# Kernel tuning notes

Hardware: AMD Instinct MI355X
Metric: run time of the kernel (lower is better)

The kernel has to match this reference:

```python
import jax, jax.numpy as jnp
import numpy as np

B, NUM_RX, NUM_CHIRPS, SAMPLES = 16, 4, 64, 256
D_BINS, R_BINS = 64, 256


def _conv3d(x, w, b, pad):
    y = jax.lax.conv_general_dilated(x, w, (1, 1, 1), pad,
                                     dimension_numbers=('NCDHW', 'OIDHW', 'NCDHW'))
    return y + b[None, :, None, None, None]


def _conv2d(x, w, b, pad):
    y = jax.lax.conv_general_dilated(x, w, (1, 1), pad,
                                     dimension_numbers=('NCHW', 'OIHW', 'NCHW'))
    return y + b[None, :, None, None]


def _bn2(x, s, t):
    return x * s[None, :, None, None] + t[None, :, None, None]


def _bn3(x, s, t):
    return x * s[None, :, None, None, None] + t[None, :, None, None, None]


def _upsample_bilinear_ac(x, oh, ow):
    # torch Upsample(mode='bilinear', align_corners=True)
    _, _, h, w = x.shape
    ph = jnp.linspace(0.0, h - 1.0, oh)
    pw = jnp.linspace(0.0, w - 1.0, ow)
    h0 = jnp.clip(jnp.floor(ph).astype(jnp.int32), 0, h - 1)
    h1 = jnp.clip(h0 + 1, 0, h - 1)
    fh = ph - h0
    w0 = jnp.clip(jnp.floor(pw).astype(jnp.int32), 0, w - 1)
    w1 = jnp.clip(w0 + 1, 0, w - 1)
    fw = pw - w0
    x = x[:, :, h0, :] * (1.0 - fh)[None, None, :, None] + x[:, :, h1, :] * fh[None, None, :, None]
    x = x[:, :, :, w0] * (1.0 - fw) + x[:, :, :, w1] * fw
    return x


def setup_inputs() -> dict:
    ks = iter(jax.random.split(jax.random.key(0), 80))

    def nrm(shape, s=0.05):
        return s * jax.random.normal(next(ks), shape, dtype=jnp.float32)

    inp = {'x': jax.random.normal(next(ks), (B, NUM_RX, NUM_CHIRPS, SAMPLES, 2), dtype=jnp.float32)}

    def conv(name, shape):
        inp[name + '_w'] = nrm(shape)
        inp[name + '_b'] = nrm((shape[0],))

    def bn(name, n):  # BatchNorm in inference form folded to scale/shift
        inp[name + '_s'] = 1.0 + nrm((n,), 0.1)
        inp[name + '_t'] = nrm((n,), 0.1)

    conv('tc1', (16, 2, 1, 1, 3)); bn('tc1', 16)
    conv('tc2', (32, 16, 1, 1, 3)); bn('tc2', 32)
    conv('rx', (32, 32, NUM_RX, 1, 1)); bn('rx', 32)
    conv('cc1', (64, 32 * NUM_CHIRPS, 3, 3)); bn('cc1', 64)
    conv('cc2', (64, 64, 3, 3)); bn('cc2', 64)
    conv('rd1', (128, 64, 3, 3)); bn('rd1', 128)
    conv('rd2', (128, 128, 3, 3)); bn('rd2', 128)
    conv('up1', (64, 128, 3, 3)); bn('up1', 64)
    conv('up2', (32, 64, 3, 3)); bn('up2', 32)
    conv('up3', (1, 32, 1, 1))
    inp['wr'] = jax.random.normal(next(ks), (SAMPLES, R_BINS, 2), dtype=jnp.float32)
    inp['wd'] = jax.random.normal(next(ks), (NUM_CHIRPS, D_BINS, 2), dtype=jnp.float32)
    return inp


def reference(x, tc1_w, tc1_b, tc1_s, tc1_t, tc2_w, tc2_b, tc2_s, tc2_t,
              rx_w, rx_b, rx_s, rx_t, cc1_w, cc1_b, cc1_s, cc1_t,
              cc2_w, cc2_b, cc2_s, cc2_t, rd1_w, rd1_b, rd1_s, rd1_t,
              rd2_w, rd2_b, rd2_s, rd2_t, up1_w, up1_b, up1_s, up1_t,
              up2_w, up2_b, up2_s, up2_t, up3_w, up3_b, wr, wd):
    r = jax.nn.relu
    p3 = [(0, 0), (0, 0), (1, 1)]
    p2 = [(1, 1), (1, 1)]
    h = jnp.transpose(x, (0, 4, 1, 2, 3))                      # [B,2,RX,C,S]
    h = r(_bn3(_conv3d(h, tc1_w, tc1_b, p3), tc1_s, tc1_t))
    h = r(_bn3(_conv3d(h, tc2_w, tc2_b, p3), tc2_s, tc2_t))
    h = r(_bn3(_conv3d(h, rx_w, rx_b, [(0, 0)] * 3), rx_s, rx_t))[:, :, 0]  # [B,32,C,S]
    h = h.reshape(h.shape[0], -1, SAMPLES)[:, :, None, :]      # [B,32*C,1,S]
    h = r(_bn2(_conv2d(h, cc1_w, cc1_b, p2), cc1_s, cc1_t))
    h = r(_bn2(_conv2d(h, cc2_w, cc2_b, p2), cc2_s, cc2_t))
    h = r(_bn2(_conv2d(h, rd1_w, rd1_b, p2), rd1_s, rd1_t))
    h = r(_bn2(_conv2d(h, rd2_w, rd2_b, p2), rd2_s, rd2_t))
    h = _upsample_bilinear_ac(h, D_BINS, R_BINS)               # [B,128,D,R]
    h = r(_bn2(_conv2d(h, up1_w, up1_b, p2), up1_s, up1_t))
    h = r(_bn2(_conv2d(h, up2_w, up2_b, p2), up2_s, up2_t))
    h = jax.nn.sigmoid(_conv2d(h, up3_w, up3_b, [(0, 0), (0, 0)]))  # [B,1,D,R]
    # learnable_fft (input is real: x_imag = 0), loops -> two batched matmuls
    xr = h[:, 0]                                               # [B,D,R]
    rr = jnp.einsum('bcs,sr->bcr', xr, wr[:, :, 0])            # range DFT, real
    ri = jnp.einsum('bcs,sr->bcr', xr, wr[:, :, 1])            # range DFT, imag
    rdr = jnp.einsum('bcr,cd->bdr', rr, wd[:, :, 0]) - jnp.einsum('bcr,cd->bdr', ri, wd[:, :, 1])
    rdi = jnp.einsum('bcr,cd->bdr', rr, wd[:, :, 1]) + jnp.einsum('bcr,cd->bdr', ri, wd[:, :, 0])
    mag = jnp.sqrt(rdr * rdr + rdi * rdi) / (NUM_CHIRPS * SAMPLES)
    out = jnp.clip(h + 0.1 * mag[:, None], 0.0, 1.0)
    return jnp.transpose(out, (0, 2, 3, 1))                    # [B,D,R,1]
```

## Files before the change

kernel.cpp:

```cpp
#include <hip/hip_runtime.h>
#include <math.h>

#define OFF_A      0u
#define OFF_P      8388608u
#define OFF_WCC1   10485760u
#define OFF_BCC1   11010048u
#define OFF_WCC2   11010112u
#define OFF_BCC2   11026496u
#define OFF_WRD1   11026560u
#define OFF_BRD1   11059328u
#define OFF_WRD2   11059456u
#define OFF_BRD2   11124992u
#define OFF_WUP1   11125120u
#define OFF_BUP1   11223424u
#define OFF_WUP2   11223488u
#define OFF_BUP2   11346368u
#define OFF_WRX    11346400u
#define OFF_W1F    11350496u
#define OFF_B1F    11350592u
#define OFF_W2F    11350608u
#define OFF_B2F    11352144u
#define OFF_BRXF   11352176u
#define OFF_RP0    0u
#define OFF_RP1    524288u
#define OFF_H      1048576u

__device__ __forceinline__ void fma4(float4& a, const float4& x, float w) {
  a.x = fmaf(x.x, w, a.x); a.y = fmaf(x.y, w, a.y);
  a.z = fmaf(x.z, w, a.z); a.w = fmaf(x.w, w, a.w);
}

__global__ __launch_bounds__(256) void k_repack_front(
    const float* __restrict__ tc1_w, const float* __restrict__ tc1_b, const float* __restrict__ tc1_s, const float* __restrict__ tc1_t,
    const float* __restrict__ tc2_w, const float* __restrict__ tc2_b, const float* __restrict__ tc2_s, const float* __restrict__ tc2_t,
    const float* __restrict__ rx_w, const float* __restrict__ rx_b, const float* __restrict__ rx_s, const float* __restrict__ rx_t,
    float* __restrict__ ws)
{
  const int tid = blockIdx.x * blockDim.x + threadIdx.x;
  const int nth = gridDim.x * blockDim.x;
  for (int i = tid; i < 96; i += nth) ws[OFF_W1F + i] = tc1_w[i] * tc1_s[i/6];
  for (int i = tid; i < 16; i += nth) ws[OFF_B1F + i] = tc1_b[i]*tc1_s[i] + tc1_t[i];
  for (int i = tid; i < 1536; i += nth) {
    int oc = i & 31, r = i >> 5, k = r % 3, ic = r / 3;
    ws[OFF_W2F + i] = tc2_w[oc*48 + ic*3 + k] * tc2_s[oc];
  }
  for (int i = tid; i < 32; i += nth) ws[OFF_B2F + i] = tc2_b[i]*tc2_s[i] + tc2_t[i];
  for (int i = tid; i < 4096; i += nth) {
    int oc = i & 31, ic = (i >> 5) & 31, rxi = i >> 10;
    ws[OFF_WRX + i] = rx_w[(oc*32 + ic)*4 + rxi] * rx_s[oc];
  }
  for (int i = tid; i < 32; i += nth) ws[OFF_BRXF + i] = rx_b[i]*rx_s[i] + rx_t[i];
}

__global__ __launch_bounds__(256, 4) void k_front(
    const float* __restrict__ x, const float* __restrict__ ws_c, float* __restrict__ ws,
    const float* __restrict__ cc1_w, const float* __restrict__ cc1_b, const float* __restrict__ cc1_s, const float* __restrict__ cc1_t,
    const float* __restrict__ cc2_w, const float* __restrict__ cc2_b, const float* __restrict__ cc2_s, const float* __restrict__ cc2_t,
    const float* __restrict__ rd1_w, const float* __restrict__ rd1_b, const float* __restrict__ rd1_s, const float* __restrict__ rd1_t,
    const float* __restrict__ rd2_w, const float* __restrict__ rd2_b, const float* __restrict__ rd2_s, const float* __restrict__ rd2_t,
    const float* __restrict__ up1_w, const float* __restrict__ up1_b, const float* __restrict__ up1_s, const float* __restrict__ up1_t,
    const float* __restrict__ up2_w, const float* __restrict__ up2_b, const float* __restrict__ up2_s, const float* __restrict__ up2_t,
    float* __restrict__ A)
{
  __shared__ float t1s[16][258];
  const int tid = threadIdx.x;

  if (blockIdx.x < 64) {
    const int t = blockIdx.x * 256 + tid;
    const int nth = 64 * 256;
    for (int i = t; i < 2048*64*4; i += nth) {
      int k = i & 3, oc = (i >> 2) & 63, c2 = i >> 8;
      ws[OFF_WCC1 + i] = (k < 3) ? cc1_w[((oc*2048 + c2)*3 + 1)*3 + k] * cc1_s[oc] : 0.f;
    }
    for (int i = t; i < 64; i += nth) ws[OFF_BCC1 + i] = cc1_b[i]*cc1_s[i] + cc1_t[i];
    for (int i = t; i < 64*64; i += nth) {
      int oc = i & 63, ic = i >> 6;
      float4 v;
      v.x = cc2_w[(oc*64 + ic)*9 + 3] * cc2_s[oc];
      v.y = cc2_w[(oc*64 + ic)*9 + 4] * cc2_s[oc];
      v.z = cc2_w[(oc*64 + ic)*9 + 5] * cc2_s[oc];
      v.w = 0.f;
      ((float4*)(ws + OFF_WCC2))[i] = v;
    }
    for (int i = t; i < 64; i += nth) ws[OFF_BCC2 + i] = cc2_b[i]*cc2_s[i] + cc2_t[i];
    for (int i = t; i < 64*128; i += nth) {
      int oc = i & 127, ic = i >> 7;
      float4 v;
      v.x = rd1_w[(oc*64 + ic)*9 + 3] * rd1_s[oc];
      v.y = rd1_w[(oc*64 + ic)*9 + 4] * rd1_s[oc];
      v.z = rd1_w[(oc*64 + ic)*9 + 5] * rd1_s[oc];
      v.w = 0.f;
      ((float4*)(ws + OFF_WRD1))[i] = v;
    }
    for (int i = t; i < 128; i += nth) ws[OFF_BRD1 + i] = rd1_b[i]*rd1_s[i] + rd1_t[i];
    for (int i = t; i < 128*128; i += nth) {
      int oc = i & 127, ic = i >> 7;
      float4 v;
      v.x = rd2_w[(oc*128 + ic)*9 + 3] * rd2_s[oc];
      v.y = rd2_w[(oc*128 + ic)*9 + 4] * rd2_s[oc];
      v.z = rd2_w[(oc*128 + ic)*9 + 5] * rd2_s[oc];
      v.w = 0.f;
      ((float4*)(ws + OFF_WRD2))[i] = v;
    }
    for (int i = t; i < 128; i += nth) ws[OFF_BRD2 + i] = rd2_b[i]*rd2_s[i] + rd2_t[i];
    for (int i = t; i < 3*128*64; i += nth) {
      int oc = i & 63, ic = (i >> 6) & 127, v = i >> 13;
      const int m = (v == 0) ? 6 : (v == 1) ? 7 : 3;
      float4 o = make_float4(0.f, 0.f, 0.f, 0.f);
      for (int kh = 0; kh < 3; ++kh)
        if ((m >> kh) & 1) {
          o.x += up1_w[((oc*128 + ic)*3 + kh)*3 + 0];
          o.y += up1_w[((oc*128 + ic)*3 + kh)*3 + 1];
          o.z += up1_w[((oc*128 + ic)*3 + kh)*3 + 2];
        }
      o.x *= up1_s[oc]; o.y *= up1_s[oc]; o.z *= up1_s[oc];
      ((float4*)(ws + OFF_WUP1))[i] = o;
    }
    for (int i = t; i < 64; i += nth) ws[OFF_BUP1 + i] = up1_b[i]*up1_s[i] + up1_t[i];
    for (int i = t; i < 5*3*64*32; i += nth) {
      int oc = i & 31, ic = (i >> 5) & 63, tt = i >> 11;
      int src = tt % 3, v = tt / 3;
      const int MASKS[15] = {2,4,0,  1,6,0,  0,7,0,  0,3,4,  0,1,2};
      const int m = MASKS[v*3 + src];
      float4 o = make_float4(0.f, 0.f, 0.f, 0.f);
      for (int kh = 0; kh < 3; ++kh)
        if ((m >> kh) & 1) {
          o.x += up2_w[((oc*64 + ic)*3 + kh)*3 + 0];
          o.y += up2_w[((oc*64 + ic)*3 + kh)*3 + 1];
          o.z += up2_w[((oc*64 + ic)*3 + kh)*3 + 2];
        }
      o.x *= up2_s[oc]; o.y *= up2_s[oc]; o.z *= up2_s[oc];
      ((float4*)(ws + OFF_WUP2))[i] = o;
    }
    for (int i = t; i < 32; i += nth) ws[OFF_BUP2 + i] = up2_b[i]*up2_s[i] + up2_t[i];
    return;
  }

  const int bb = blockIdx.x - 64;
  const int b = bb >> 6, chirp = bb & 63;
  const int s = tid;

  if (tid < 32) { int o = tid & 15; int c = (tid >> 4) ? 257 : 0; t1s[o][c] = 0.f; }

  const float* w1f  = ws_c + OFF_W1F;
  const float* b1f  = ws_c + OFF_B1F;
  const float* w2f  = ws_c + OFF_W2F;
  const float* b2f  = ws_c + OFF_B2F;
  const float* wrxf = ws_c + OFF_WRX;
  const float* brxf = ws_c + OFF_BRXF;

  float acc[32];
  #pragma unroll
  for (int j = 0; j < 32; ++j) acc[j] = 0.f;

  #pragma unroll 1
  for (int rxi = 0; rxi < 4; ++rxi) {
    {
      const float2* xb2 = (const float2*)(x + ((size_t)(((b*4 + rxi)*64 + chirp)*256) << 1));
      float2 xm = xb2[s];
      float2 xl = xb2[(s == 0) ? 0 : (s - 1)];
      float2 xr = xb2[(s == 255) ? 255 : (s + 1)];
      if (s == 0)   { xl.x = 0.f; xl.y = 0.f; }
      if (s == 255) { xr.x = 0.f; xr.y = 0.f; }
      #pragma unroll 4
      for (int o = 0; o < 16; ++o) {
        const float* w = w1f + o*6;
        float v = b1f[o];
        v = fmaf(xl.x, w[0], v);
        v = fmaf(xm.x, w[1], v);
        v = fmaf(xr.x, w[2], v);
        v = fmaf(xl.y, w[3], v);
        v = fmaf(xm.y, w[4], v);
        v = fmaf(xr.y, w[5], v);
        t1s[o][s+1] = fmaxf(v, 0.f);
      }
    }
    __syncthreads();

    float t2[32];
    #pragma unroll
    for (int j = 0; j < 32; ++j) t2[j] = b2f[j];
    #pragma unroll 2
    for (int ic = 0; ic < 16; ++ic) {
      float tl = t1s[ic][s];
      float tm = t1s[ic][s+1];
      float tr = t1s[ic][s+2];
      const float* w = w2f + ic*96;
      #pragma unroll
      for (int oc = 0; oc < 32; ++oc)
        t2[oc] = fmaf(tl, w[oc], fmaf(tm, w[32+oc], fmaf(tr, w[64+oc], t2[oc])));
    }
    #pragma unroll
    for (int j = 0; j < 32; ++j) t2[j] = fmaxf(t2[j], 0.f);

    const float* wr0 = wrxf + rxi*1024;
    #pragma unroll 4
    for (int ic = 0; ic < 32; ++ic) {
      float tv = t2[ic];
      const float* w = wr0 + ic*32;
      #pragma unroll
      for (int oc = 0; oc < 32; ++oc)
        acc[oc] = fmaf(tv, w[oc], acc[oc]);
    }
    __syncthreads();
  }

  #pragma unroll 4
  for (int oc = 0; oc < 32; ++oc) {
    float v = fmaxf(acc[oc] + brxf[oc], 0.f);
    A[(size_t)((b*2048 + oc*64 + chirp)*256) + s] = v;
  }
}

__global__ __launch_bounds__(256) void k_cc1(
    const float* __restrict__ A, const float* __restrict__ wp, float* __restrict__ P)
{
  __shared__ __align__(16) float As[256][36];
  const int tid = threadIdx.x;
  const int ks = blockIdx.x & 7;
  const int stile = (blockIdx.x >> 3) & 7;
  const int b = blockIdx.x >> 6;
  const int s0 = stile * 32;
  const int oc = tid & 63;
  const int sg = tid >> 6;
  const int cbase = ks * 256;
  const float4* w4 = (const float4*)wp;

  for (int i = tid; i < 256*36; i += 256) {
    int c = i / 36, si = i - c*36;
    int sA = s0 - 1 + si;
    float v = 0.f;
    if (si < 34 && sA >= 0 && sA < 256)
      v = A[(size_t)(b*2048 + cbase + c)*256 + sA];
    As[c][si] = v;
  }
  __syncthreads();

  const int sb = sg * 8;
  float4 acc0 = make_float4(0.f,0.f,0.f,0.f);
  float4 acc1 = make_float4(0.f,0.f,0.f,0.f);
  #pragma unroll 4
  for (int c = 0; c < 256; ++c) {
    float4 w = w4[(size_t)(cbase + c)*64 + oc];
    float4 a0 = *(const float4*)&As[c][sb];
    float4 a1 = *(const float4*)&As[c][sb + 4];
    float2 a2 = *(const float2*)&As[c][sb + 8];
    acc0.x = fmaf(a0.x,w.x, fmaf(a0.y,w.y, fmaf(a0.z,w.z, acc0.x)));
    acc0.y = fmaf(a0.y,w.x, fmaf(a0.z,w.y, fmaf(a0.w,w.z, acc0.y)));
    acc0.z = fmaf(a0.z,w.x, fmaf(a0.w,w.y, fmaf(a1.x,w.z, acc0.z)));
    acc0.w = fmaf(a0.w,w.x, fmaf(a1.x,w.y, fmaf(a1.y,w.z, acc0.w)));
    acc1.x = fmaf(a1.x,w.x, fmaf(a1.y,w.y, fmaf(a1.z,w.z, acc1.x)));
    acc1.y = fmaf(a1.y,w.x, fmaf(a1.z,w.y, fmaf(a1.w,w.z, acc1.y)));
    acc1.z = fmaf(a1.z,w.x, fmaf(a1.w,w.y, fmaf(a2.x,w.z, acc1.z)));
    acc1.w = fmaf(a1.w,w.x, fmaf(a2.x,w.y, fmaf(a2.y,w.z, acc1.w)));
  }
  float* Pk = P + ((size_t)(ks*16 + b)*256)*64;
  int s = s0 + sb;
  Pk[(size_t)(s+0)*64 + oc] = acc0.x;
  Pk[(size_t)(s+1)*64 + oc] = acc0.y;
  Pk[(size_t)(s+2)*64 + oc] = acc0.z;
  Pk[(size_t)(s+3)*64 + oc] = acc0.w;
  Pk[(size_t)(s+4)*64 + oc] = acc1.x;
  Pk[(size_t)(s+5)*64 + oc] = acc1.y;
  Pk[(size_t)(s+6)*64 + oc] = acc1.z;
  Pk[(size_t)(s+7)*64 + oc] = acc1.w;
}

__global__ __launch_bounds__(256) void k_mid(
    const float* __restrict__ P, const float* __restrict__ bcc1,
    const float* __restrict__ wcc2, const float* __restrict__ bcc2,
    const float* __restrict__ wrd1, const float* __restrict__ brd1,
    const float* __restrict__ wrd2, const float* __restrict__ brd2,
    float* __restrict__ Rp0, float* __restrict__ Rp1)
{
  __shared__ __align__(16) float c1s[64][20];
  __shared__ __align__(16) float c2s[64][20];
  __shared__ __align__(16) float r1s[64][12];
  const int tid = threadIdx.x;
  const int half = blockIdx.x & 1;
  const int stile = (blockIdx.x >> 1) & 31;
  const int b = blockIdx.x >> 6;
  const int s0 = stile * 8;
  const float4* wc2 = (const float4*)wcc2;
  const float4* wr1 = (const float4*)wrd1;
  const float4* wr2 = (const float4*)wrd2;

  for (int i = tid; i < 14*64; i += 256) {
    int ic = i & 63, si = i >> 6;
    int sA = s0 - 3 + si;
    float v = 0.f;
    if (sA >= 0 && sA < 256) {
      float a = bcc1[ic];
      #pragma unroll
      for (int ksp = 0; ksp < 8; ++ksp)
        a += P[((size_t)(ksp*16 + b)*256 + sA)*64 + ic];
      v = fmaxf(a, 0.f);
    }
    c1s[ic][si] = v;
  }
  __syncthreads();

  {
    const int g = tid >> 6, oc = tid & 63;
    if (g < 3) {
      float bb = bcc2[oc];
      float4 acc = make_float4(bb, bb, bb, bb);
      #pragma unroll 4
      for (int ic = 0; ic < 64; ++ic) {
        float4 w = wc2[ic*64 + oc];
        float4 ca = *(const float4*)&c1s[ic][g*4];
        float2 cb = *(const float2*)&c1s[ic][g*4 + 4];
        acc.x = fmaf(ca.x,w.x, fmaf(ca.y,w.y, fmaf(ca.z,w.z, acc.x)));
        acc.y = fmaf(ca.y,w.x, fmaf(ca.z,w.y, fmaf(ca.w,w.z, acc.y)));
        acc.z = fmaf(ca.z,w.x, fmaf(ca.w,w.y, fmaf(cb.x,w.z, acc.z)));
        acc.w = fmaf(ca.w,w.x, fmaf(cb.x,w.y, fmaf(cb.y,w.z, acc.w)));
      }
      float r[4] = {acc.x, acc.y, acc.z, acc.w};
      #pragma unroll
      for (int j = 0; j < 4; ++j) {
        int si = g*4 + j, sA = s0 - 2 + si;
        c2s[oc][si] = (sA >= 0 && sA < 256) ? fmaxf(r[j], 0.f) : 0.f;
      }
    } else {
      int oc2 = tid - 192;
      c2s[oc2][12] = 0.f;
      c2s[oc2][13] = 0.f;
    }
  }
  __syncthreads();

  {
    const int g = tid >> 6, ocl = tid & 63;
    if (g < 3) {
      const int ocg = half*64 + ocl;
      float bb = brd1[ocg];
      float4 acc = make_float4(bb, bb, bb, bb);
      #pragma unroll 4
      for (int ic = 0; ic < 64; ++ic) {
        float4 w = wr1[ic*128 + ocg];
        float4 ca = *(const float4*)&c2s[ic][g*4];
        float2 cb = *(const float2*)&c2s[ic][g*4 + 4];
        acc.x = fmaf(ca.x,w.x, fmaf(ca.y,w.y, fmaf(ca.z,w.z, acc.x)));
        acc.y = fmaf(ca.y,w.x, fmaf(ca.z,w.y, fmaf(ca.w,w.z, acc.y)));
        acc.z = fmaf(ca.z,w.x, fmaf(ca.w,w.y, fmaf(cb.x,w.z, acc.z)));
        acc.w = fmaf(ca.w,w.x, fmaf(cb.x,w.y, fmaf(cb.y,w.z, acc.w)));
      }
      float r[4] = {acc.x, acc.y, acc.z, acc.w};
      #pragma unroll
      for (int j = 0; j < 4; ++j) {
        int si = g*4 + j, sA = s0 - 1 + si;
        if (si < 10)
          r1s[ocl][si] = (sA >= 0 && sA < 256) ? fmaxf(r[j], 0.f) : 0.f;
      }
    } else {
      int oc2 = tid - 192;
      r1s[oc2][10] = 0.f;
      r1s[oc2][11] = 0.f;
    }
  }
  __syncthreads();

  {
    const int g = tid >> 7, oc = tid & 127;
    float bb = half ? 0.f : brd2[oc];
    float4 acc = make_float4(bb, bb, bb, bb);
    #pragma unroll 4
    for (int ic = 0; ic < 64; ++ic) {
      float4 w = wr2[(half*64 + ic)*128 + oc];
      float4 ca = *(const float4*)&r1s[ic][g*4];
      float2 cb = *(const float2*)&r1s[ic][g*4 + 4];
      acc.x = fmaf(ca.x,w.x, fmaf(ca.y,w.y, fmaf(ca.z,w.z, acc.x)));
      acc.y = fmaf(ca.y,w.x, fmaf(ca.z,w.y, fmaf(ca.w,w.z, acc.y)));
      acc.z = fmaf(ca.z,w.x, fmaf(ca.w,w.y, fmaf(cb.x,w.z, acc.z)));
      acc.w = fmaf(ca.w,w.x, fmaf(cb.x,w.y, fmaf(cb.y,w.z, acc.w)));
    }
    float* Rp = half ? Rp1 : Rp0;
    int s = s0 + g*4;
    Rp[((size_t)b*256 + s+0)*128 + oc] = acc.x;
    Rp[((size_t)b*256 + s+1)*128 + oc] = acc.y;
    Rp[((size_t)b*256 + s+2)*128 + oc] = acc.z;
    Rp[((size_t)b*256 + s+3)*128 + oc] = acc.w;
  }
}

__global__ __launch_bounds__(192) void k_up(
    const float* __restrict__ Rp0, const float* __restrict__ Rp1,
    const float* __restrict__ wup1, const float* __restrict__ bup1,
    const float* __restrict__ wup2, const float* __restrict__ bup2,
    const float* __restrict__ up3_w, const float* __restrict__ up3_b,
    float* __restrict__ H)
{
  __shared__ __align__(16) float Rs[128][12];
  __shared__ __align__(16) float u1s[3][64][12];
  __shared__ float u2s[5][32][9];
  const int tid = threadIdx.x;
  const int b = blockIdx.x >> 5;
  const int s0 = (blockIdx.x & 31) * 8;

  for (int i = tid; i < 128*12; i += 192) {
    int ic = i & 127, si = i >> 7;
    int sA = s0 - 2 + si;
    float v = 0.f;
    if (sA >= 0 && sA < 256) {
      size_t idx = ((size_t)b*256 + sA)*128 + ic;
      v = fmaxf(Rp0[idx] + Rp1[idx], 0.f);
    }
    Rs[ic][si] = v;
  }
  __syncthreads();

  {
    const int vi = tid >> 6, oc = tid & 63;
    const float4* w4 = (const float4*)wup1;
    float a[10];
    float bb = bup1[oc];
    #pragma unroll
    for (int p = 0; p < 10; ++p) a[p] = bb;
    #pragma unroll 4
    for (int ic = 0; ic < 128; ++ic) {
      float4 w = w4[(vi*128 + ic)*64 + oc];
      float4 ra = *(const float4*)&Rs[ic][0];
      float4 rb = *(const float4*)&Rs[ic][4];
      float4 rc = *(const float4*)&Rs[ic][8];
      float r[12] = {ra.x,ra.y,ra.z,ra.w, rb.x,rb.y,rb.z,rb.w, rc.x,rc.y,rc.z,rc.w};
      #pragma unroll
      for (int p = 0; p < 10; ++p)
        a[p] = fmaf(r[p],w.x, fmaf(r[p+1],w.y, fmaf(r[p+2],w.z, a[p])));
    }
    #pragma unroll
    for (int p = 0; p < 10; ++p) {
      int sA = s0 - 1 + p;
      u1s[vi][oc][p] = (sA >= 0 && sA < 256) ? fmaxf(a[p], 0.f) : 0.f;
    }
    u1s[vi][oc][10] = 0.f; u1s[vi][oc][11] = 0.f;
  }
  __syncthreads();

  if (tid < 160) {
    const int v = tid >> 5, oc = tid & 31;
    const float4* w4 = (const float4*)wup2;
    float a[8];
    float bb = bup2[oc];
    #pragma unroll
    for (int p = 0; p < 8; ++p) a[p] = bb;
    for (int src = 0; src < 3; ++src) {
      #pragma unroll 4
      for (int ic = 0; ic < 64; ++ic) {
        float4 w = w4[((v*3 + src)*64 + ic)*32 + oc];
        float4 ua = *(const float4*)&u1s[src][ic][0];
        float4 ub = *(const float4*)&u1s[src][ic][4];
        float2 uc = *(const float2*)&u1s[src][ic][8];
        float r[10] = {ua.x,ua.y,ua.z,ua.w, ub.x,ub.y,ub.z,ub.w, uc.x,uc.y};
        #pragma unroll
        for (int p = 0; p < 8; ++p)
          a[p] = fmaf(r[p],w.x, fmaf(r[p+1],w.y, fmaf(r[p+2],w.z, a[p])));
      }
    }
    #pragma unroll
    for (int p = 0; p < 8; ++p) u2s[v][oc][p] = fmaxf(a[p], 0.f);
  }
  __syncthreads();

  if (tid < 40) {
    int v = tid >> 3, j = tid & 7;
    float a = up3_b[0];
    for (int ic = 0; ic < 32; ++ic)
      a = fmaf(u2s[v][ic][j], up3_w[ic], a);
    H[(size_t)(b*5 + v)*256 + s0 + j] = 1.f / (1.f + expf(-a));
  }
}

__global__ __launch_bounds__(256) void k_spec(
    const float* __restrict__ H, const float* __restrict__ wr, const float* __restrict__ wd,
    float* __restrict__ out)
{
  __shared__ float hs[5][256];
  __shared__ float S0[64], S1[64];
  __shared__ float wds[4][64][2];
  __shared__ float ps[16][16][10];
  __shared__ float rred[16][10];
  const int tid = threadIdx.x;
  const int b = blockIdx.x >> 4;
  const int rt = blockIdx.x & 15;
  const int r0 = rt * 16;

  for (int i = tid; i < 1280; i += 256) hs[i >> 8][i & 255] = H[(size_t)b*1280 + i];
  if (tid < 64) {
    const float2* wd2 = (const float2*)wd;
    float a0 = 0.f, a1 = 0.f;
    for (int c = 2; c <= 61; ++c) {
      float2 v = wd2[c*64 + tid];
      a0 += v.x; a1 += v.y;
    }
    S0[tid] = a0; S1[tid] = a1;
  }
  for (int i = tid; i < 512; i += 256) {
    int row = i >> 7, rem = i & 127, d = rem >> 1, comp = rem & 1;
    int c = (row < 2) ? row : (60 + row);
    wds[row][d][comp] = wd[(c*64 + d)*2 + comp];
  }
  __syncthreads();

  {
    const int rl = tid & 15;
    const int sq = tid >> 4;
    const int r = r0 + rl;
    float rr[5] = {0,0,0,0,0}, ri[5] = {0,0,0,0,0};
    const float2* wr2p = (const float2*)wr;
    for (int s = sq*16; s < sq*16 + 16; ++s) {
      float2 w = wr2p[s*256 + r];
      #pragma unroll
      for (int k = 0; k < 5; ++k) {
        float hv = hs[k][s];
        rr[k] = fmaf(hv, w.x, rr[k]);
        ri[k] = fmaf(hv, w.y, ri[k]);
      }
    }
    #pragma unroll
    for (int k = 0; k < 5; ++k) {
      ps[sq][rl][k]     = rr[k];
      ps[sq][rl][5 + k] = ri[k];
    }
  }
  __syncthreads();

  if (tid < 160) {
    const int rl = tid & 15, k = tid >> 4;
    float a = 0.f;
    #pragma unroll
    for (int sq = 0; sq < 16; ++sq) a += ps[sq][rl][k];
    rred[rl][k] = a;
  }
  __syncthreads();

  {
    const int rl = tid & 15, dg = tid >> 4;
    const int r = r0 + rl;
    float Rr[5], Ri[5];
    #pragma unroll
    for (int k = 0; k < 5; ++k) { Rr[k] = rred[rl][k]; Ri[k] = rred[rl][5 + k]; }
    for (int dd = 0; dd < 4; ++dd) {
      int d = dg*4 + dd;
      float w0r = wds[0][d][0], w0i = wds[0][d][1];
      float w1r = wds[1][d][0], w1i = wds[1][d][1];
      float w2r = wds[2][d][0], w2i = wds[2][d][1];
      float w3r = wds[3][d][0], w3i = wds[3][d][1];
      float s0v = S0[d], s1v = S1[d];
      float rdr = Rr[0]*w0r + Rr[1]*w1r + Rr[2]*s0v + Rr[3]*w2r + Rr[4]*w3r
                - Ri[0]*w0i - Ri[1]*w1i - Ri[2]*s1v - Ri[3]*w2i - Ri[4]*w3i;
      float rdi = Rr[0]*w0i + Rr[1]*w1i + Rr[2]*s1v + Rr[3]*w2i + Rr[4]*w3i
                + Ri[0]*w0r + Ri[1]*w1r + Ri[2]*s0v + Ri[3]*w2r + Ri[4]*w3r;
      float mag = sqrtf(rdr*rdr + rdi*rdi) * (1.0f / 16384.0f);
      int v = (d == 0) ? 0 : (d == 1) ? 1 : (d <= 61) ? 2 : ((d == 62) ? 3 : 4);
      float o = hs[v][r] + 0.1f * mag;
      out[(size_t)b*16384 + d*256 + r] = fminf(fmaxf(o, 0.f), 1.f);
    }
  }
}

extern "C" void kernel_launch(void* const* d_in, const int* in_sizes, int n_in,
                              void* d_out, int out_size, void* d_ws, size_t ws_size,
                              hipStream_t stream)
{
  const float* x     = (const float*)d_in[0];
  const float* tc1_w = (const float*)d_in[1];  const float* tc1_b = (const float*)d_in[2];
  const float* tc1_s = (const float*)d_in[3];  const float* tc1_t = (const float*)d_in[4];
  const float* tc2_w = (const float*)d_in[5];  const float* tc2_b = (const float*)d_in[6];
  const float* tc2_s = (const float*)d_in[7];  const float* tc2_t = (const float*)d_in[8];
  const float* rx_w  = (const float*)d_in[9];  const float* rx_b  = (const float*)d_in[10];
  const float* rx_s  = (const float*)d_in[11]; const float* rx_t  = (const float*)d_in[12];
  const float* cc1_w = (const float*)d_in[13]; const float* cc1_b = (const float*)d_in[14];
  const float* cc1_s = (const float*)d_in[15]; const float* cc1_t = (const float*)d_in[16];
  const float* cc2_w = (const float*)d_in[17]; const float* cc2_b = (const float*)d_in[18];
  const float* cc2_s = (const float*)d_in[19]; const float* cc2_t = (const float*)d_in[20];
  const float* rd1_w = (const float*)d_in[21]; const float* rd1_b = (const float*)d_in[22];
  const float* rd1_s = (const float*)d_in[23]; const float* rd1_t = (const float*)d_in[24];
  const float* rd2_w = (const float*)d_in[25]; const float* rd2_b = (const float*)d_in[26];
  const float* rd2_s = (const float*)d_in[27]; const float* rd2_t = (const float*)d_in[28];
  const float* up1_w = (const float*)d_in[29]; const float* up1_b = (const float*)d_in[30];
  const float* up1_s = (const float*)d_in[31]; const float* up1_t = (const float*)d_in[32];
  const float* up2_w = (const float*)d_in[33]; const float* up2_b = (const float*)d_in[34];
  const float* up2_s = (const float*)d_in[35]; const float* up2_t = (const float*)d_in[36];
  const float* up3_w = (const float*)d_in[37]; const float* up3_b = (const float*)d_in[38];
  const float* wr    = (const float*)d_in[39];
  const float* wd    = (const float*)d_in[40];
  float* ws  = (float*)d_ws;
  float* out = (float*)d_out;

  k_repack_front<<<8, 256, 0, stream>>>(tc1_w, tc1_b, tc1_s, tc1_t,
                                        tc2_w, tc2_b, tc2_s, tc2_t,
                                        rx_w, rx_b, rx_s, rx_t, ws);
  k_front<<<1088, 256, 0, stream>>>(x, ws, ws,
                                    cc1_w, cc1_b, cc1_s, cc1_t,
                                    cc2_w, cc2_b, cc2_s, cc2_t,
                                    rd1_w, rd1_b, rd1_s, rd1_t,
                                    rd2_w, rd2_b, rd2_s, rd2_t,
                                    up1_w, up1_b, up1_s, up1_t,
                                    up2_w, up2_b, up2_s, up2_t,
                                    ws + OFF_A);
  k_cc1<<<1024, 256, 0, stream>>>(ws + OFF_A, ws + OFF_WCC1, ws + OFF_P);
  k_mid<<<1024, 256, 0, stream>>>(ws + OFF_P, ws + OFF_BCC1,
                                  ws + OFF_WCC2, ws + OFF_BCC2,
                                  ws + OFF_WRD1, ws + OFF_BRD1,
                                  ws + OFF_WRD2, ws + OFF_BRD2,
                                  ws + OFF_RP0, ws + OFF_RP1);
  k_up<<<512, 192, 0, stream>>>(ws + OFF_RP0, ws + OFF_RP1,
                                ws + OFF_WUP1, ws + OFF_BUP1,
                                ws + OFF_WUP2, ws + OFF_BUP2,
                                up3_w, up3_b, ws + OFF_H);
  k_spec<<<256, 256, 0, stream>>>(ws + OFF_H, wr, wd, out);
}
```

Measured before the change: 338.5 us.

## Halve per-block tiles in cc1, up and spec kernels; precompute Doppler sums once

The cc1, up and spec kernels now use smaller spatial tiles (16, 4 and 8 columns instead of 32, 8 and 16), which doubles their grid sizes to spread work across more CUs. cc1 also gets a higher occupancy hint. The per-block summation of Doppler weights over chirps 2..61 in k_spec moves into the repack kernel and is stored once in the workspace. The trade-off is more halo recomputation and redundant loads per output, especially in k_up, where the 2-column halos now cover proportionally more of each tile.

```diff
diff --git a/kernel.cpp b/kernel.cpp
--- a/kernel.cpp
+++ b/kernel.cpp
@@ -21,6 +21,7 @@
 #define OFF_W2F    11350608u
 #define OFF_B2F    11352144u
 #define OFF_BRXF   11352176u
+#define OFF_S01    11352208u
 #define OFF_RP0    0u
 #define OFF_RP1    524288u
 #define OFF_H      1048576u
@@ -34,6 +35,7 @@
     const float* __restrict__ tc1_w, const float* __restrict__ tc1_b, const float* __restrict__ tc1_s, const float* __restrict__ tc1_t,
     const float* __restrict__ tc2_w, const float* __restrict__ tc2_b, const float* __restrict__ tc2_s, const float* __restrict__ tc2_t,
     const float* __restrict__ rx_w, const float* __restrict__ rx_b, const float* __restrict__ rx_s, const float* __restrict__ rx_t,
+    const float* __restrict__ wd,
     float* __restrict__ ws)
 {
   const int tid = blockIdx.x * blockDim.x + threadIdx.x;
@@ -50,6 +52,12 @@
     ws[OFF_WRX + i] = rx_w[(oc*32 + ic)*4 + rxi] * rx_s[oc];
   }
   for (int i = tid; i < 32; i += nth) ws[OFF_BRXF + i] = rx_b[i]*rx_s[i] + rx_t[i];
+  for (int i = tid; i < 128; i += nth) {
+    int d = i & 63, comp = i >> 6;
+    float a = 0.f;
+    for (int c = 2; c <= 61; ++c) a += wd[(c*64 + d)*2 + comp];
+    ws[OFF_S01 + comp*64 + d] = a;
+  }
 }
 
 __global__ __launch_bounds__(256, 4) void k_front(
@@ -212,58 +220,48 @@
   }
 }
 
-__global__ __launch_bounds__(256) void k_cc1(
+__global__ __launch_bounds__(256, 8) void k_cc1(
     const float* __restrict__ A, const float* __restrict__ wp, float* __restrict__ P)
 {
-  __shared__ __align__(16) float As[256][36];
+  __shared__ __align__(16) float As[256][20];
   const int tid = threadIdx.x;
   const int ks = blockIdx.x & 7;
-  const int stile = (blockIdx.x >> 3) & 7;
-  const int b = blockIdx.x >> 6;
-  const int s0 = stile * 32;
+  const int stile = (blockIdx.x >> 3) & 15;
+  const int b = blockIdx.x >> 7;
+  const int s0 = stile * 16;
   const int oc = tid & 63;
   const int sg = tid >> 6;
   const int cbase = ks * 256;
   const float4* w4 = (const float4*)wp;
 
-  for (int i = tid; i < 256*36; i += 256) {
-    int c = i / 36, si = i - c*36;
+  for (int i = tid; i < 256*20; i += 256) {
+    int c = i / 20, si = i - c*20;
     int sA = s0 - 1 + si;
     float v = 0.f;
-    if (si < 34 && sA >= 0 && sA < 256)
+    if (si < 18 && sA >= 0 && sA < 256)
       v = A[(size_t)(b*2048 + cbase + c)*256 + sA];
     As[c][si] = v;
   }
   __syncthreads();
 
-  const int sb = sg * 8;
-  float4 acc0 = make_float4(0.f,0.f,0.f,0.f);
-  float4 acc1 = make_float4(0.f,0.f,0.f,0.f);
-  #pragma unroll 4
+  const int sb = sg * 4;
+  float4 acc = make_float4(0.f,0.f,0.f,0.f);
+  #pragma unroll 8
   for (int c = 0; c < 256; ++c) {
     float4 w = w4[(size_t)(cbase + c)*64 + oc];
     float4 a0 = *(const float4*)&As[c][sb];
-    float4 a1 = *(const float4*)&As[c][sb + 4];
-    float2 a2 = *(const float2*)&As[c][sb + 8];
-    acc0.x = fmaf(a0.x,w.x, fmaf(a0.y,w.y, fmaf(a0.z,w.z, acc0.x)));
-    acc0.y = fmaf(a0.y,w.x, fmaf(a0.z,w.y, fmaf(a0.w,w.z, acc0.y)));
-    acc0.z = fmaf(a0.z,w.x, fmaf(a0.w,w.y, fmaf(a1.x,w.z, acc0.z)));
-    acc0.w = fmaf(a0.w,w.x, fmaf(a1.x,w.y, fmaf(a1.y,w.z, acc0.w)));
-    acc1.x = fmaf(a1.x,w.x, fmaf(a1.y,w.y, fmaf(a1.z,w.z, acc1.x)));
-    acc1.y = fmaf(a1.y,w.x, fmaf(a1.z,w.y, fmaf(a1.w,w.z, acc1.y)));
-    acc1.z = fmaf(a1.z,w.x, fmaf(a1.w,w.y, fmaf(a2.x,w.z, acc1.z)));
-    acc1.w = fmaf(a1.w,w.x, fmaf(a2.x,w.y, fmaf(a2.y,w.z, acc1.w)));
+    float2 a1 = *(const float2*)&As[c][sb + 4];
+    acc.x = fmaf(a0.x,w.x, fmaf(a0.y,w.y, fmaf(a0.z,w.z, acc.x)));
+    acc.y = fmaf(a0.y,w.x, fmaf(a0.z,w.y, fmaf(a0.w,w.z, acc.y)));
+    acc.z = fmaf(a0.z,w.x, fmaf(a0.w,w.y, fmaf(a1.x,w.z, acc.z)));
+    acc.w = fmaf(a0.w,w.x, fmaf(a1.x,w.y, fmaf(a1.y,w.z, acc.w)));
   }
   float* Pk = P + ((size_t)(ks*16 + b)*256)*64;
   int s = s0 + sb;
-  Pk[(size_t)(s+0)*64 + oc] = acc0.x;
-  Pk[(size_t)(s+1)*64 + oc] = acc0.y;
-  Pk[(size_t)(s+2)*64 + oc] = acc0.z;
-  Pk[(size_t)(s+3)*64 + oc] = acc0.w;
-  Pk[(size_t)(s+4)*64 + oc] = acc1.x;
-  Pk[(size_t)(s+5)*64 + oc] = acc1.y;
-  Pk[(size_t)(s+6)*64 + oc] = acc1.z;
-  Pk[(size_t)(s+7)*64 + oc] = acc1.w;
+  Pk[(size_t)(s+0)*64 + oc] = acc.x;
+  Pk[(size_t)(s+1)*64 + oc] = acc.y;
+  Pk[(size_t)(s+2)*64 + oc] = acc.z;
+  Pk[(size_t)(s+3)*64 + oc] = acc.w;
 }
 
 __global__ __launch_bounds__(256) void k_mid(
@@ -390,15 +388,15 @@
     const float* __restrict__ up3_w, const float* __restrict__ up3_b,
     float* __restrict__ H)
 {
-  __shared__ __align__(16) float Rs[128][12];
-  __shared__ __align__(16) float u1s[3][64][12];
-  __shared__ float u2s[5][32][9];
+  __shared__ __align__(16) float Rs[128][8];
+  __shared__ __align__(16) float u1s[3][64][8];
+  __shared__ float u2s[5][32][5];
   const int tid = threadIdx.x;
-  const int b = blockIdx.x >> 5;
-  const int s0 = (blockIdx.x & 31) * 8;
-
-  for (int i = tid; i < 128*12; i += 192) {
-    int ic = i & 127, si = i >> 7;
+  const int b = blockIdx.x >> 6;
+  const int s0 = (blockIdx.x & 63) * 4;
+
+  for (int i = tid; i < 128*8; i += 192) {
+    int ic = i >> 3, si = i & 7;
     int sA = s0 - 2 + si;
     float v = 0.f;
     if (sA >= 0 && sA < 256) {
@@ -412,57 +410,55 @@
   {
     const int vi = tid >> 6, oc = tid & 63;
     const float4* w4 = (const float4*)wup1;
-    float a[10];
+    float a[6];
     float bb = bup1[oc];
     #pragma unroll
-    for (int p = 0; p < 10; ++p) a[p] = bb;
+    for (int p = 0; p < 6; ++p) a[p] = bb;
     #pragma unroll 4
     for (int ic = 0; ic < 128; ++ic) {
       float4 w = w4[(vi*128 + ic)*64 + oc];
       float4 ra = *(const float4*)&Rs[ic][0];
       float4 rb = *(const float4*)&Rs[ic][4];
-      float4 rc = *(const float4*)&Rs[ic][8];
-      float r[12] = {ra.x,ra.y,ra.z,ra.w, rb.x,rb.y,rb.z,rb.w, rc.x,rc.y,rc.z,rc.w};
+      float r[8] = {ra.x,ra.y,ra.z,ra.w, rb.x,rb.y,rb.z,rb.w};
       #pragma unroll
-      for (int p = 0; p < 10; ++p)
+      for (int p = 0; p < 6; ++p)
         a[p] = fmaf(r[p],w.x, fmaf(r[p+1],w.y, fmaf(r[p+2],w.z, a[p])));
     }
     #pragma unroll
-    for (int p = 0; p < 10; ++p) {
+    for (int p = 0; p < 6; ++p) {
       int sA = s0 - 1 + p;
       u1s[vi][oc][p] = (sA >= 0 && sA < 256) ? fmaxf(a[p], 0.f) : 0.f;
     }
-    u1s[vi][oc][10] = 0.f; u1s[vi][oc][11] = 0.f;
+    u1s[vi][oc][6] = 0.f; u1s[vi][oc][7] = 0.f;
   }
   __syncthreads();
 
   if (tid < 160) {
     const int v = tid >> 5, oc = tid & 31;
     const float4* w4 = (const float4*)wup2;
-    float a[8];
+    float a[4];
     float bb = bup2[oc];
     #pragma unroll
-    for (int p = 0; p < 8; ++p) a[p] = bb;
+    for (int p = 0; p < 4; ++p) a[p] = bb;
     for (int src = 0; src < 3; ++src) {
       #pragma unroll 4
       for (int ic = 0; ic < 64; ++ic) {
         float4 w = w4[((v*3 + src)*64 + ic)*32 + oc];
         float4 ua = *(const float4*)&u1s[src][ic][0];
-        float4 ub = *(const float4*)&u1s[src][ic][4];
-        float2 uc = *(const float2*)&u1s[src][ic][8];
-        float r[10] = {ua.x,ua.y,ua.z,ua.w, ub.x,ub.y,ub.z,ub.w, uc.x,uc.y};
+        float2 ub = *(const float2*)&u1s[src][ic][4];
+        float r[6] = {ua.x,ua.y,ua.z,ua.w, ub.x,ub.y};
         #pragma unroll
-        for (int p = 0; p < 8; ++p)
+        for (int p = 0; p < 4; ++p)
           a[p] = fmaf(r[p],w.x, fmaf(r[p+1],w.y, fmaf(r[p+2],w.z, a[p])));
       }
     }
     #pragma unroll
-    for (int p = 0; p < 8; ++p) u2s[v][oc][p] = fmaxf(a[p], 0.f);
-  }
-  __syncthreads();
-
-  if (tid < 40) {
-    int v = tid >> 3, j = tid & 7;
+    for (int p = 0; p < 4; ++p) u2s[v][oc][p] = fmaxf(a[p], 0.f);
+  }
+  __syncthreads();
+
+  if (tid < 20) {
+    int v = tid >> 2, j = tid & 3;
     float a = up3_b[0];
     for (int ic = 0; ic < 32; ++ic)
       a = fmaf(u2s[v][ic][j], up3_w[ic], a);
@@ -472,27 +468,23 @@
 
 __global__ __launch_bounds__(256) void k_spec(
     const float* __restrict__ H, const float* __restrict__ wr, const float* __restrict__ wd,
-    float* __restrict__ out)
+    const float* __restrict__ S01, float* __restrict__ out)
 {
   __shared__ float hs[5][256];
   __shared__ float S0[64], S1[64];
   __shared__ float wds[4][64][2];
-  __shared__ float ps[16][16][10];
-  __shared__ float rred[16][10];
+  __shared__ float ps[32][8][10];
+  __shared__ float rred[8][10];
   const int tid = threadIdx.x;
-  const int b = blockIdx.x >> 4;
-  const int rt = blockIdx.x & 15;
-  const int r0 = rt * 16;
+  const int b = blockIdx.x >> 5;
+  const int rt = blockIdx.x & 31;
+  const int r0 = rt * 8;
 
   for (int i = tid; i < 1280; i += 256) hs[i >> 8][i & 255] = H[(size_t)b*1280 + i];
-  if (tid < 64) {
-    const float2* wd2 = (const float2*)wd;
-    float a0 = 0.f, a1 = 0.f;
-    for (int c = 2; c <= 61; ++c) {
-      float2 v = wd2[c*64 + tid];
-      a0 += v.x; a1 += v.y;
-    }
-    S0[tid] = a0; S1[tid] = a1;
+  if (tid < 128) {
+    int comp = tid >> 6, d = tid & 63;
+    float v = S01[comp*64 + d];
+    if (comp) S1[d] = v; else S0[d] = v;
   }
   for (int i = tid; i < 512; i += 256) {
     int row = i >> 7, rem = i & 127, d = rem >> 1, comp = rem & 1;
@@ -502,12 +494,12 @@
   __syncthreads();
 
   {
-    const int rl = tid & 15;
-    const int sq = tid >> 4;
+    const int rl = tid & 7;
+    const int sq = tid >> 3;
     const int r = r0 + rl;
     float rr[5] = {0,0,0,0,0}, ri[5] = {0,0,0,0,0};
     const float2* wr2p = (const float2*)wr;
-    for (int s = sq*16; s < sq*16 + 16; ++s) {
+    for (int s = sq*8; s < sq*8 + 8; ++s) {
       float2 w = wr2p[s*256 + r];
       #pragma unroll
       for (int k = 0; k < 5; ++k) {
@@ -524,23 +516,23 @@
   }
   __syncthreads();
 
-  if (tid < 160) {
-    const int rl = tid & 15, k = tid >> 4;
+  if (tid < 80) {
+    const int rl = tid & 7, k = tid >> 3;
     float a = 0.f;
     #pragma unroll
-    for (int sq = 0; sq < 16; ++sq) a += ps[sq][rl][k];
+    for (int sq = 0; sq < 32; ++sq) a += ps[sq][rl][k];
     rred[rl][k] = a;
   }
   __syncthreads();
 
   {
-    const int rl = tid & 15, dg = tid >> 4;
+    const int rl = tid & 7, dg = tid >> 3;
     const int r = r0 + rl;
     float Rr[5], Ri[5];
     #pragma unroll
     for (int k = 0; k < 5; ++k) { Rr[k] = rred[rl][k]; Ri[k] = rred[rl][5 + k]; }
-    for (int dd = 0; dd < 4; ++dd) {
-      int d = dg*4 + dd;
+    for (int dd = 0; dd < 2; ++dd) {
+      int d = dg*2 + dd;
       float w0r = wds[0][d][0], w0i = wds[0][d][1];
       float w1r = wds[1][d][0], w1i = wds[1][d][1];
       float w2r = wds[2][d][0], w2i = wds[2][d][1];
@@ -589,7 +581,7 @@
 
   k_repack_front<<<8, 256, 0, stream>>>(tc1_w, tc1_b, tc1_s, tc1_t,
                                         tc2_w, tc2_b, tc2_s, tc2_t,
-                                        rx_w, rx_b, rx_s, rx_t, ws);
+                                        rx_w, rx_b, rx_s, rx_t, wd, ws);
   k_front<<<1088, 256, 0, stream>>>(x, ws, ws,
                                     cc1_w, cc1_b, cc1_s, cc1_t,
                                     cc2_w, cc2_b, cc2_s, cc2_t,
@@ -598,15 +590,15 @@
                                     up1_w, up1_b, up1_s, up1_t,
                                     up2_w, up2_b, up2_s, up2_t,
                                     ws + OFF_A);
-  k_cc1<<<1024, 256, 0, stream>>>(ws + OFF_A, ws + OFF_WCC1, ws + OFF_P);
+  k_cc1<<<2048, 256, 0, stream>>>(ws + OFF_A, ws + OFF_WCC1, ws + OFF_P);
   k_mid<<<1024, 256, 0, stream>>>(ws + OFF_P, ws + OFF_BCC1,
                                   ws + OFF_WCC2, ws + OFF_BCC2,
                                   ws + OFF_WRD1, ws + OFF_BRD1,
                                   ws + OFF_WRD2, ws + OFF_BRD2,
                                   ws + OFF_RP0, ws + OFF_RP1);
-  k_up<<<512, 192, 0, stream>>>(ws + OFF_RP0, ws + OFF_RP1,
-                                ws + OFF_WUP1, ws + OFF_BUP1,
-                                ws + OFF_WUP2, ws + OFF_BUP2,
-                                up3_w, up3_b, ws + OFF_H);
-  k_spec<<<256, 256, 0, stream>>>(ws + OFF_H, wr, wd, out);
-}
+  k_up<<<1024, 192, 0, stream>>>(ws + OFF_RP0, ws + OFF_RP1,
+                                 ws + OFF_WUP1, ws + OFF_BUP1,
+                                 ws + OFF_WUP2, ws + OFF_BUP2,
+                                 up3_w, up3_b, ws + OFF_H);
+  k_spec<<<512, 256, 0, stream>>>(ws + OFF_H, wr, wd, ws + OFF_S01, out);
+}
```

New measurement: 382.5 us. 13.0% more time.
